# Optimization experiments

Hardware: AMD Instinct MI355X
Metric: run time of the kernel (lower is better)

## Reference

```python
import jax, jax.numpy as jnp
import numpy as np

N_NODES = 1024
N_EDGES = 32768
FEAT = 384
HID = 64
OUT = 64


def setup_inputs() -> dict:
    key = jax.random.key(0)
    ks = jax.random.split(key, 10)
    features = jax.random.normal(ks[0], (N_NODES, FEAT), dtype=jnp.float32)
    edge_index = jax.random.randint(ks[1], (2, N_EDGES), 0, N_NODES, dtype=jnp.int64 if jax.config.jax_enable_x64 else jnp.int32)
    edge_attr = jax.random.uniform(ks[2], (N_EDGES, 1), dtype=jnp.float32)
    # Linear weights (stored as [in, out]; torch Linear does x @ W.T)
    sc = 1.0 / np.sqrt(FEAT)
    Wk = jax.random.uniform(ks[3], (FEAT, HID), dtype=jnp.float32, minval=-sc, maxval=sc)
    Wq = jax.random.uniform(ks[4], (FEAT, HID), dtype=jnp.float32, minval=-sc, maxval=sc)
    Wv = jax.random.uniform(ks[5], (FEAT, OUT), dtype=jnp.float32, minval=-sc, maxval=sc)
    # Embedding tables, init N(0, 1)
    Ek = jax.random.normal(ks[6], (2, HID), dtype=jnp.float32)
    Eq = jax.random.normal(ks[7], (2, HID), dtype=jnp.float32)
    Ev = jax.random.normal(ks[8], (2, OUT), dtype=jnp.float32)
    bias = jnp.full((1,), 0.5, dtype=jnp.float32)
    mult = jnp.full((1,), 10.0, dtype=jnp.float32)
    return {"features": features, "edge_index": edge_index, "edge_attr": edge_attr,
            "Wk": Wk, "Wq": Wq, "Wv": Wv, "Ek": Ek, "Eq": Eq, "Ev": Ev,
            "bias": bias, "mult": mult}


def _dense_adj(src, dst, vals, n, d):
    # torch_geometric.utils.to_dense_adj: scatter-add edge attrs into [N, N, d]
    return jnp.zeros((n, n, d), vals.dtype).at[src, dst].add(vals)


def reference(features, edge_index, edge_attr, Wk, Wq, Wv, Ek, Eq, Ev, bias, mult):
    N, L = features.shape
    k = features @ Wk                      # [N, H]
    q = features @ Wq                      # [N, H]
    v = features @ Wv                      # [N, O]

    # ContinuousEmbeddingIndex: sigmoid interp, weights [E, 2]
    w = jax.nn.sigmoid((edge_attr - bias) * mult)
    w = jnp.concatenate([w, 1.0 - w], axis=-1)

    src, dst = edge_index[0], edge_index[1]
    A = q @ k.T                            # [N, N]

    # key relative embeddings (original casts to int64 -> truncate toward 0)
    rk = jnp.trunc(w @ Ek)                 # [E, H]
    Rk = _dense_adj(src, dst, rk, N, Ek.shape[1])
    A = A + jnp.einsum('ih,ijh->ij', q, Rk)

    # query relative embeddings (also truncated)
    rq = jnp.trunc(w @ Eq)
    Rq = _dense_adj(src, dst, rq, N, Eq.shape[1])
    A = A + jnp.einsum('jh,ijh->ij', k, Rq)

    # term3: (q_repeat * k_repeat).sum(-1) == q @ k.T again
    A = A + q @ k.T

    A = jax.nn.softmax(A / jnp.sqrt(jnp.asarray(L, A.dtype)), axis=-1)
    # dropout is identity at inference
    M = A @ v

    # value relative embeddings (float, no truncation)
    rv = w @ Ev                            # [E, O]
    Rv = _dense_adj(src, dst, rv, N, Ev.shape[1])
    M = M + jnp.einsum('ij,ijd->id', A, Rv)
    return M
```

## Files before the change

kernel.cpp:

```cpp
#include <hip/hip_runtime.h>
#include <math.h>

#define N_NODES 1024
#define N_EDGES 32768
#define FEAT    384
#define INV_S   0.05103103630798287f

__global__ __launch_bounds__(384) void k_kqv(
        const float* __restrict__ feat,
        const float* __restrict__ Wk, const float* __restrict__ Wq,
        const float* __restrict__ Wv,
        float* __restrict__ q, float* __restrict__ k, float* __restrict__ v) {
    __shared__ float fs[4 * FEAT];
    const int tid = threadIdx.x;
    const int row0 = blockIdx.x * 4;
    ((float4*)fs)[tid] = ((const float4*)(feat + (size_t)row0 * FEAT))[tid];
    __syncthreads();
    const int mat = tid >> 7;
    const int sub = tid & 127;
    const int col = sub & 63;
    const int rh  = sub >> 6;
    const float* W  = (mat == 0) ? Wq : (mat == 1 ? Wk : Wv);
    const float* f0 = fs + (rh * 2) * FEAT;
    const float* f1 = fs + (rh * 2 + 1) * FEAT;
    float a0 = 0.f, a1 = 0.f;
    #pragma unroll 8
    for (int f = 0; f < FEAT; ++f) {
        float wv = W[f * 64 + col];
        a0 = fmaf(f0[f], wv, a0);
        a1 = fmaf(f1[f], wv, a1);
    }
    float* out = (mat == 0) ? q : (mat == 1 ? k : v);
    out[(row0 + rh * 2 + 0) * 64 + col] = a0;
    out[(row0 + rh * 2 + 1) * 64 + col] = a1;
}

__global__ __launch_bounds__(256) void k_qkt(
        const float* __restrict__ q, const float* __restrict__ k,
        float* __restrict__ A) {
    __shared__ float qs[64][65];
    __shared__ float kst[64][65];
    const int tid = threadIdx.x;
    const int rowbase = blockIdx.y * 64, colbase = blockIdx.x * 64;
    for (int idx = tid; idx < 4096; idx += 256) {
        int r = idx >> 6, c = idx & 63;
        qs[r][c] = q[(rowbase + r) * 64 + c];
        kst[c][r] = k[(colbase + r) * 64 + c];
    }
    __syncthreads();
    const int tx = tid & 15, ty = tid >> 4;
    float acc[4][4] = {};
    for (int kk = 0; kk < 64; ++kk) {
        float a0 = qs[ty * 4 + 0][kk], a1 = qs[ty * 4 + 1][kk];
        float a2 = qs[ty * 4 + 2][kk], a3 = qs[ty * 4 + 3][kk];
        float b0 = kst[kk][tx * 4 + 0], b1 = kst[kk][tx * 4 + 1];
        float b2 = kst[kk][tx * 4 + 2], b3 = kst[kk][tx * 4 + 3];
        acc[0][0] = fmaf(a0, b0, acc[0][0]); acc[0][1] = fmaf(a0, b1, acc[0][1]);
        acc[0][2] = fmaf(a0, b2, acc[0][2]); acc[0][3] = fmaf(a0, b3, acc[0][3]);
        acc[1][0] = fmaf(a1, b0, acc[1][0]); acc[1][1] = fmaf(a1, b1, acc[1][1]);
        acc[1][2] = fmaf(a1, b2, acc[1][2]); acc[1][3] = fmaf(a1, b3, acc[1][3]);
        acc[2][0] = fmaf(a2, b0, acc[2][0]); acc[2][1] = fmaf(a2, b1, acc[2][1]);
        acc[2][2] = fmaf(a2, b2, acc[2][2]); acc[2][3] = fmaf(a2, b3, acc[2][3]);
        acc[3][0] = fmaf(a3, b0, acc[3][0]); acc[3][1] = fmaf(a3, b1, acc[3][1]);
        acc[3][2] = fmaf(a3, b2, acc[3][2]); acc[3][3] = fmaf(a3, b3, acc[3][3]);
    }
    for (int i = 0; i < 4; ++i) {
        float4 o = make_float4(2.f * acc[i][0], 2.f * acc[i][1],
                               2.f * acc[i][2], 2.f * acc[i][3]);
        *(float4*)&A[(size_t)(rowbase + ty * 4 + i) * N_NODES + colbase + tx * 4] = o;
    }
}

__global__ __launch_bounds__(256) void k_edgeA(
        const int* __restrict__ ei, const float* __restrict__ eattr,
        const float* __restrict__ Ek, const float* __restrict__ Eq,
        const float* __restrict__ q, const float* __restrict__ k,
        const float* __restrict__ bias, const float* __restrict__ mult,
        float* __restrict__ A) {
    const int e = (blockIdx.x * 256 + threadIdx.x) >> 6;
    const int lane = threadIdx.x & 63;
    const int src = ei[e], dst = ei[N_EDGES + e];
    const float w  = 1.0f / (1.0f + expf(-(eattr[e] - bias[0]) * mult[0]));
    const float w1 = 1.0f - w;
    const float rk = truncf(w * Ek[lane] + w1 * Ek[64 + lane]);
    const float rq = truncf(w * Eq[lane] + w1 * Eq[64 + lane]);
    float c = q[src * 64 + lane] * rk + k[dst * 64 + lane] * rq;
    #pragma unroll
    for (int off = 32; off >= 1; off >>= 1) c += __shfl_xor(c, off, 64);
    if (lane == 0) atomicAdd(&A[(size_t)src * N_NODES + dst], c);
}

__global__ __launch_bounds__(256) void k_avsm(
        const float* __restrict__ A, const float* __restrict__ v,
        float* __restrict__ rowstats, float* __restrict__ M) {
    __shared__ float As[2][1024];
    __shared__ __align__(16) float chunk[128 * 68];
    __shared__ float redm[4], reds[4];
    __shared__ float red[2][2][64];
    const int tid  = threadIdx.x;
    const int lane = tid & 63;
    const int wave = tid >> 6;
    const int row0 = blockIdx.x * 2;

    #pragma unroll
    for (int i = 0; i < 2; ++i) {
        const int idx = tid + i * 256;
        ((float4*)As)[idx] = ((const float4*)(A + (size_t)row0 * N_NODES))[idx];
    }
    __syncthreads();

    const int g  = tid >> 7;
    const int lt = tid & 127;
    {
        float4 x0 = *(float4*)&As[g][lt * 8];
        float4 x1 = *(float4*)&As[g][lt * 8 + 4];
        float m = fmaxf(fmaxf(fmaxf(x0.x, x0.y), fmaxf(x0.z, x0.w)),
                        fmaxf(fmaxf(x1.x, x1.y), fmaxf(x1.z, x1.w)));
        #pragma unroll
        for (int off = 32; off >= 1; off >>= 1) m = fmaxf(m, __shfl_xor(m, off, 64));
        if (lane == 0) redm[wave] = m;
        __syncthreads();
        m = fmaxf(redm[g * 2], redm[g * 2 + 1]);
        float e0 = expf((x0.x - m) * INV_S), e1 = expf((x0.y - m) * INV_S);
        float e2 = expf((x0.z - m) * INV_S), e3 = expf((x0.w - m) * INV_S);
        float e4 = expf((x1.x - m) * INV_S), e5 = expf((x1.y - m) * INV_S);
        float e6 = expf((x1.z - m) * INV_S), e7 = expf((x1.w - m) * INV_S);
        float s = ((e0 + e1) + (e2 + e3)) + ((e4 + e5) + (e6 + e7));
        #pragma unroll
        for (int off = 32; off >= 1; off >>= 1) s += __shfl_xor(s, off, 64);
        if (lane == 0) reds[wave] = s;
        __syncthreads();
        s = reds[g * 2] + reds[g * 2 + 1];
        const float rs = 1.0f / s;
        if (lt == 0) {
            rowstats[(row0 + g) * 2 + 0] = m;
            rowstats[(row0 + g) * 2 + 1] = rs;
        }
        *(float4*)&As[g][lt * 8]     = make_float4(e0 * rs, e1 * rs, e2 * rs, e3 * rs);
        *(float4*)&As[g][lt * 8 + 4] = make_float4(e4 * rs, e5 * rs, e6 * rs, e7 * rs);
    }
    __syncthreads();

    const int r = wave >> 1, h = wave & 1, d = lane;
    float acc = 0.f;
    for (int ch = 0; ch < 8; ++ch) {
        const int jb = ch * 128;
        #pragma unroll
        for (int it = 0; it < 8; ++it) {
            const int idx = tid + it * 256;
            const int j = idx >> 4, d4 = (idx & 15) * 4;
            *(float4*)&chunk[j * 68 + d4] =
                *(const float4*)&v[(size_t)(jb + j) * 64 + d4];
        }
        __syncthreads();
        const float* as = &As[r][jb + h * 64];
        const float* ck = &chunk[h * 64 * 68 + d];
        #pragma unroll 8
        for (int j = 0; j < 64; ++j)
            acc = fmaf(as[j], ck[j * 68], acc);
        __syncthreads();
    }
    red[r][h][d] = acc;
    __syncthreads();
    if (tid < 128) {
        const int rr = tid >> 6, dd = tid & 63;
        M[(row0 + rr) * 64 + dd] = red[rr][0][dd] + red[rr][1][dd];
    }
}

__global__ __launch_bounds__(256) void k_edgeM(
        const int* __restrict__ ei, const float* __restrict__ eattr,
        const float* __restrict__ Ev, const float* __restrict__ bias,
        const float* __restrict__ mult,
        const float* __restrict__ A, const float* __restrict__ rowstats,
        float* __restrict__ M) {
    const int e = (blockIdx.x * 256 + threadIdx.x) >> 6;
    const int lane = threadIdx.x & 63;
    const int src = ei[e], dst = ei[N_EDGES + e];
    const float logit = A[(size_t)src * N_NODES + dst];
    const float m  = rowstats[src * 2 + 0];
    const float rs = rowstats[src * 2 + 1];
    const float prob = expf((logit - m) * INV_S) * rs;
    const float w = 1.0f / (1.0f + expf(-(eattr[e] - bias[0]) * mult[0]));
    const float rv = w * Ev[lane] + (1.0f - w) * Ev[64 + lane];
    atomicAdd(&M[src * 64 + lane], prob * rv);
}

extern "C" void kernel_launch(void* const* d_in, const int* in_sizes, int n_in,
                              void* d_out, int out_size, void* d_ws, size_t ws_size,
                              hipStream_t stream) {
    (void)in_sizes; (void)n_in; (void)out_size; (void)ws_size;
    const float* feat  = (const float*)d_in[0];
    const int*   ei    = (const int*)d_in[1];
    const float* eattr = (const float*)d_in[2];
    const float* Wk    = (const float*)d_in[3];
    const float* Wq    = (const float*)d_in[4];
    const float* Wv    = (const float*)d_in[5];
    const float* Ek    = (const float*)d_in[6];
    const float* Eq    = (const float*)d_in[7];
    const float* Ev    = (const float*)d_in[8];
    const float* bias  = (const float*)d_in[9];
    const float* mult  = (const float*)d_in[10];
    float* M = (float*)d_out;

    float* wsf = (float*)d_ws;
    float* q        = wsf;
    float* k        = wsf + 65536;
    float* v        = wsf + 131072;
    float* A        = wsf + 196608;
    float* rowstats = wsf + 196608 + 1048576;

    k_kqv<<<256, 384, 0, stream>>>(feat, Wk, Wq, Wv, q, k, v);
    k_qkt<<<dim3(16, 16), 256, 0, stream>>>(q, k, A);
    k_edgeA<<<8192, 256, 0, stream>>>(ei, eattr, Ek, Eq, q, k, bias, mult, A);
    k_avsm<<<512, 256, 0, stream>>>(A, v, rowstats, M);
    k_edgeM<<<8192, 256, 0, stream>>>(ei, eattr, Ev, bias, mult, A, rowstats, M);
}
```

Before: 128.6 us.

## Factor value-embedding term into per-row scalars and restructure softmax/AV pipeline

Measured after the change: 132.2 us. 2.8% more time.

```diff
diff --git a/kernel.cpp b/kernel.cpp
--- a/kernel.cpp
+++ b/kernel.cpp
@@ -77,113 +77,130 @@
         const float* __restrict__ q, const float* __restrict__ k,
         const float* __restrict__ bias, const float* __restrict__ mult,
         float* __restrict__ A) {
-    const int e = (blockIdx.x * 256 + threadIdx.x) >> 6;
     const int lane = threadIdx.x & 63;
-    const int src = ei[e], dst = ei[N_EDGES + e];
-    const float w  = 1.0f / (1.0f + expf(-(eattr[e] - bias[0]) * mult[0]));
-    const float w1 = 1.0f - w;
-    const float rk = truncf(w * Ek[lane] + w1 * Ek[64 + lane]);
-    const float rq = truncf(w * Eq[lane] + w1 * Eq[64 + lane]);
-    float c = q[src * 64 + lane] * rk + k[dst * 64 + lane] * rq;
+    const int gw   = blockIdx.x * 4 + (threadIdx.x >> 6);
+    const float b0 = bias[0], mu = mult[0];
+    const float ek0 = Ek[lane], ek1 = Ek[64 + lane];
+    const float eq0 = Eq[lane], eq1 = Eq[64 + lane];
+    #pragma unroll 2
+    for (int i = 0; i < 4; ++i) {
+        const int e = gw + i * 8192;
+        const int src = ei[e], dst = ei[N_EDGES + e];
+        const float w  = 1.0f / (1.0f + expf(-(eattr[e] - b0) * mu));
+        const float rk = truncf(w * ek0 + (1.0f - w) * ek1);
+        const float rq = truncf(w * eq0 + (1.0f - w) * eq1);
+        float c = q[src * 64 + lane] * rk + k[dst * 64 + lane] * rq;
+        #pragma unroll
+        for (int off = 32; off >= 1; off >>= 1) c += __shfl_xor(c, off, 64);
+        if (lane == 0) atomicAdd(&A[(size_t)src * N_NODES + dst], c);
+    }
+}
+
+__global__ __launch_bounds__(256) void k_stats(
+        const float* __restrict__ A, float* __restrict__ rowstats,
+        float* __restrict__ S) {
+    const int tid = threadIdx.x, lane = tid & 63, wave = tid >> 6;
+    if (blockIdx.x == 0)
+        for (int i = tid; i < 2 * N_NODES; i += 256) S[i] = 0.f;
+    const int row = blockIdx.x * 4 + wave;
+    const float4* Ar = (const float4*)(A + (size_t)row * N_NODES);
+    float4 x0 = Ar[lane * 4 + 0], x1 = Ar[lane * 4 + 1];
+    float4 x2 = Ar[lane * 4 + 2], x3 = Ar[lane * 4 + 3];
+    float m = fmaxf(fmaxf(fmaxf(x0.x, x0.y), fmaxf(x0.z, x0.w)),
+                    fmaxf(fmaxf(x1.x, x1.y), fmaxf(x1.z, x1.w)));
+    m = fmaxf(m, fmaxf(fmaxf(fmaxf(x2.x, x2.y), fmaxf(x2.z, x2.w)),
+                       fmaxf(fmaxf(x3.x, x3.y), fmaxf(x3.z, x3.w))));
     #pragma unroll
-    for (int off = 32; off >= 1; off >>= 1) c += __shfl_xor(c, off, 64);
-    if (lane == 0) atomicAdd(&A[(size_t)src * N_NODES + dst], c);
-}
-
-__global__ __launch_bounds__(256) void k_avsm(
-        const float* __restrict__ A, const float* __restrict__ v,
-        float* __restrict__ rowstats, float* __restrict__ M) {
-    __shared__ float As[2][1024];
-    __shared__ __align__(16) float chunk[128 * 68];
-    __shared__ float redm[4], reds[4];
-    __shared__ float red[2][2][64];
-    const int tid  = threadIdx.x;
-    const int lane = tid & 63;
-    const int wave = tid >> 6;
-    const int row0 = blockIdx.x * 2;
-
+    for (int off = 32; off >= 1; off >>= 1) m = fmaxf(m, __shfl_xor(m, off, 64));
+    float s = expf((x0.x - m) * INV_S) + expf((x0.y - m) * INV_S)
+            + expf((x0.z - m) * INV_S) + expf((x0.w - m) * INV_S)
+            + expf((x1.x - m) * INV_S) + expf((x1.y - m) * INV_S)
+            + expf((x1.z - m) * INV_S) + expf((x1.w - m) * INV_S)
+            + expf((x2.x - m) * INV_S) + expf((x2.y - m) * INV_S)
+            + expf((x2.z - m) * INV_S) + expf((x2.w - m) * INV_S)
+            + expf((x3.x - m) * INV_S) + expf((x3.y - m) * INV_S)
+            + expf((x3.z - m) * INV_S) + expf((x3.w - m) * INV_S);
     #pragma unroll
-    for (int i = 0; i < 2; ++i) {
-        const int idx = tid + i * 256;
-        ((float4*)As)[idx] = ((const float4*)(A + (size_t)row0 * N_NODES))[idx];
-    }
-    __syncthreads();
-
-    const int g  = tid >> 7;
-    const int lt = tid & 127;
-    {
-        float4 x0 = *(float4*)&As[g][lt * 8];
-        float4 x1 = *(float4*)&As[g][lt * 8 + 4];
-        float m = fmaxf(fmaxf(fmaxf(x0.x, x0.y), fmaxf(x0.z, x0.w)),
-                        fmaxf(fmaxf(x1.x, x1.y), fmaxf(x1.z, x1.w)));
-        #pragma unroll
-        for (int off = 32; off >= 1; off >>= 1) m = fmaxf(m, __shfl_xor(m, off, 64));
-        if (lane == 0) redm[wave] = m;
-        __syncthreads();
-        m = fmaxf(redm[g * 2], redm[g * 2 + 1]);
-        float e0 = expf((x0.x - m) * INV_S), e1 = expf((x0.y - m) * INV_S);
-        float e2 = expf((x0.z - m) * INV_S), e3 = expf((x0.w - m) * INV_S);
-        float e4 = expf((x1.x - m) * INV_S), e5 = expf((x1.y - m) * INV_S);
-        float e6 = expf((x1.z - m) * INV_S), e7 = expf((x1.w - m) * INV_S);
-        float s = ((e0 + e1) + (e2 + e3)) + ((e4 + e5) + (e6 + e7));
-        #pragma unroll
-        for (int off = 32; off >= 1; off >>= 1) s += __shfl_xor(s, off, 64);
-        if (lane == 0) reds[wave] = s;
-        __syncthreads();
-        s = reds[g * 2] + reds[g * 2 + 1];
-        const float rs = 1.0f / s;
-        if (lt == 0) {
-            rowstats[(row0 + g) * 2 + 0] = m;
-            rowstats[(row0 + g) * 2 + 1] = rs;
-        }
-        *(float4*)&As[g][lt * 8]     = make_float4(e0 * rs, e1 * rs, e2 * rs, e3 * rs);
-        *(float4*)&As[g][lt * 8 + 4] = make_float4(e4 * rs, e5 * rs, e6 * rs, e7 * rs);
-    }
-    __syncthreads();
-
-    const int r = wave >> 1, h = wave & 1, d = lane;
-    float acc = 0.f;
-    for (int ch = 0; ch < 8; ++ch) {
-        const int jb = ch * 128;
-        #pragma unroll
-        for (int it = 0; it < 8; ++it) {
-            const int idx = tid + it * 256;
-            const int j = idx >> 4, d4 = (idx & 15) * 4;
-            *(float4*)&chunk[j * 68 + d4] =
-                *(const float4*)&v[(size_t)(jb + j) * 64 + d4];
-        }
-        __syncthreads();
-        const float* as = &As[r][jb + h * 64];
-        const float* ck = &chunk[h * 64 * 68 + d];
-        #pragma unroll 8
-        for (int j = 0; j < 64; ++j)
-            acc = fmaf(as[j], ck[j * 68], acc);
-        __syncthreads();
-    }
-    red[r][h][d] = acc;
-    __syncthreads();
-    if (tid < 128) {
-        const int rr = tid >> 6, dd = tid & 63;
-        M[(row0 + rr) * 64 + dd] = red[rr][0][dd] + red[rr][1][dd];
-    }
-}
-
-__global__ __launch_bounds__(256) void k_edgeM(
+    for (int off = 32; off >= 1; off >>= 1) s += __shfl_xor(s, off, 64);
+    if (lane == 0) {
+        rowstats[row * 2 + 0] = m;
+        rowstats[row * 2 + 1] = 1.0f / s;
+    }
+}
+
+__global__ __launch_bounds__(256) void k_edgeS(
         const int* __restrict__ ei, const float* __restrict__ eattr,
-        const float* __restrict__ Ev, const float* __restrict__ bias,
-        const float* __restrict__ mult,
         const float* __restrict__ A, const float* __restrict__ rowstats,
-        float* __restrict__ M) {
-    const int e = (blockIdx.x * 256 + threadIdx.x) >> 6;
-    const int lane = threadIdx.x & 63;
+        const float* __restrict__ bias, const float* __restrict__ mult,
+        float* __restrict__ S) {
+    const int e = blockIdx.x * 256 + threadIdx.x;
     const int src = ei[e], dst = ei[N_EDGES + e];
     const float logit = A[(size_t)src * N_NODES + dst];
     const float m  = rowstats[src * 2 + 0];
     const float rs = rowstats[src * 2 + 1];
     const float prob = expf((logit - m) * INV_S) * rs;
     const float w = 1.0f / (1.0f + expf(-(eattr[e] - bias[0]) * mult[0]));
-    const float rv = w * Ev[lane] + (1.0f - w) * Ev[64 + lane];
-    atomicAdd(&M[src * 64 + lane], prob * rv);
+    atomicAdd(&S[src * 2 + 0], prob * w);
+    atomicAdd(&S[src * 2 + 1], prob * (1.0f - w));
+}
+
+__global__ __launch_bounds__(256) void k_av(
+        const float* __restrict__ A, const float* __restrict__ v,
+        const float* __restrict__ rowstats, const float* __restrict__ S,
+        const float* __restrict__ Ev, float* __restrict__ M) {
+    __shared__ float P[2][1024];
+    __shared__ float red[2][4][64];
+    const int tid  = threadIdx.x;
+    const int lane = tid & 63;
+    const int wave = tid >> 6;
+    const int row0 = blockIdx.x * 2;
+
+    {
+        const int g  = tid >> 7;
+        const int lt = tid & 127;
+        const float m  = rowstats[(row0 + g) * 2 + 0];
+        const float rs = rowstats[(row0 + g) * 2 + 1];
+        const float4* Ar = (const float4*)(A + (size_t)(row0 + g) * N_NODES);
+        float4 x0 = Ar[lt * 2], x1 = Ar[lt * 2 + 1];
+        *(float4*)&P[g][lt * 8] = make_float4(
+            expf((x0.x - m) * INV_S) * rs, expf((x0.y - m) * INV_S) * rs,
+            expf((x0.z - m) * INV_S) * rs, expf((x0.w - m) * INV_S) * rs);
+        *(float4*)&P[g][lt * 8 + 4] = make_float4(
+            expf((x1.x - m) * INV_S) * rs, expf((x1.y - m) * INV_S) * rs,
+            expf((x1.z - m) * INV_S) * rs, expf((x1.w - m) * INV_S) * rs);
+    }
+    __syncthreads();
+
+    {
+        const float* vp = v + (size_t)(wave * 256) * 64 + lane;
+        const float* p0 = &P[0][wave * 256];
+        const float* p1 = &P[1][wave * 256];
+        float acc0 = 0.f, acc1 = 0.f;
+        #pragma unroll 2
+        for (int j4 = 0; j4 < 256; j4 += 4) {
+            float4 a0 = *(const float4*)&p0[j4];
+            float4 a1 = *(const float4*)&p1[j4];
+            float v0 = vp[(j4 + 0) * 64];
+            float v1 = vp[(j4 + 1) * 64];
+            float v2 = vp[(j4 + 2) * 64];
+            float v3 = vp[(j4 + 3) * 64];
+            acc0 = fmaf(a0.x, v0, acc0); acc0 = fmaf(a0.y, v1, acc0);
+            acc0 = fmaf(a0.z, v2, acc0); acc0 = fmaf(a0.w, v3, acc0);
+            acc1 = fmaf(a1.x, v0, acc1); acc1 = fmaf(a1.y, v1, acc1);
+            acc1 = fmaf(a1.z, v2, acc1); acc1 = fmaf(a1.w, v3, acc1);
+        }
+        red[0][wave][lane] = acc0;
+        red[1][wave][lane] = acc1;
+    }
+    __syncthreads();
+
+    if (tid < 128) {
+        const int r = tid >> 6, d = tid & 63;
+        const int row = row0 + r;
+        float acc = (red[r][0][d] + red[r][1][d]) + (red[r][2][d] + red[r][3][d]);
+        acc += S[row * 2 + 0] * Ev[d] + S[row * 2 + 1] * Ev[64 + d];
+        M[row * 64 + d] = acc;
+    }
 }
 
 extern "C" void kernel_launch(void* const* d_in, const int* in_sizes, int n_in,
@@ -209,10 +226,12 @@
     float* v        = wsf + 131072;
     float* A        = wsf + 196608;
     float* rowstats = wsf + 196608 + 1048576;
+    float* S        = rowstats + 2048;
 
     k_kqv<<<256, 384, 0, stream>>>(feat, Wk, Wq, Wv, q, k, v);
     k_qkt<<<dim3(16, 16), 256, 0, stream>>>(q, k, A);
-    k_edgeA<<<8192, 256, 0, stream>>>(ei, eattr, Ek, Eq, q, k, bias, mult, A);
-    k_avsm<<<512, 256, 0, stream>>>(A, v, rowstats, M);
-    k_edgeM<<<8192, 256, 0, stream>>>(ei, eattr, Ev, bias, mult, A, rowstats, M);
-}
+    k_edgeA<<<2048, 256, 0, stream>>>(ei, eattr, Ek, Eq, q, k, bias, mult, A);
+    k_stats<<<256, 256, 0, stream>>>(A, rowstats, S);
+    k_edgeS<<<128, 256, 0, stream>>>(ei, eattr, A, rowstats, bias, mult, S);
+    k_av<<<512, 256, 0, stream>>>(A, v, rowstats, S, Ev, M);
+}
```

## Fuse edge scatter, softmax, AV and edge-value terms into one row-block kernel

Applied to the files above, without the earlier changes.

Measured after the change: 123.8 us. 1.04x faster.

```diff
diff --git a/kernel.cpp b/kernel.cpp
--- a/kernel.cpp
+++ b/kernel.cpp
@@ -5,6 +5,7 @@
 #define N_EDGES 32768
 #define FEAT    384
 #define INV_S   0.05103103630798287f
+#define MAXH    1024
 
 __global__ __launch_bounds__(384) void k_kqv(
         const float* __restrict__ feat,
@@ -71,41 +72,73 @@
     }
 }
 
-__global__ __launch_bounds__(256) void k_edgeA(
+__global__ __launch_bounds__(512) void k_mega(
+        const float* __restrict__ A0, const float* __restrict__ q,
+        const float* __restrict__ k, const float* __restrict__ v,
         const int* __restrict__ ei, const float* __restrict__ eattr,
         const float* __restrict__ Ek, const float* __restrict__ Eq,
-        const float* __restrict__ q, const float* __restrict__ k,
+        const float* __restrict__ Ev,
         const float* __restrict__ bias, const float* __restrict__ mult,
-        float* __restrict__ A) {
-    const int e = (blockIdx.x * 256 + threadIdx.x) >> 6;
-    const int lane = threadIdx.x & 63;
-    const int src = ei[e], dst = ei[N_EDGES + e];
-    const float w  = 1.0f / (1.0f + expf(-(eattr[e] - bias[0]) * mult[0]));
-    const float w1 = 1.0f - w;
-    const float rk = truncf(w * Ek[lane] + w1 * Ek[64 + lane]);
-    const float rq = truncf(w * Eq[lane] + w1 * Eq[64 + lane]);
-    float c = q[src * 64 + lane] * rk + k[dst * 64 + lane] * rq;
-    #pragma unroll
-    for (int off = 32; off >= 1; off >>= 1) c += __shfl_xor(c, off, 64);
-    if (lane == 0) atomicAdd(&A[(size_t)src * N_NODES + dst], c);
-}
-
-__global__ __launch_bounds__(256) void k_avsm(
-        const float* __restrict__ A, const float* __restrict__ v,
-        float* __restrict__ rowstats, float* __restrict__ M) {
-    __shared__ float As[2][1024];
-    __shared__ __align__(16) float chunk[128 * 68];
-    __shared__ float redm[4], reds[4];
-    __shared__ float red[2][2][64];
+        float* __restrict__ M) {
+    __shared__ __align__(16) float As[4][N_NODES];
+    __shared__ float qr[4][64];
+    __shared__ __align__(16) float scratch[2048];
+    __shared__ float redm[8], reds[8];
+    __shared__ float sS[4][2];
+    __shared__ int nhit;
+    int*   list  = (int*)scratch;
+    float* wlist = scratch + 1024;
+    float* red   = scratch;
+
     const int tid  = threadIdx.x;
     const int lane = tid & 63;
     const int wave = tid >> 6;
-    const int row0 = blockIdx.x * 2;
-
-    #pragma unroll
-    for (int i = 0; i < 2; ++i) {
-        const int idx = tid + i * 256;
-        ((float4*)As)[idx] = ((const float4*)(A + (size_t)row0 * N_NODES))[idx];
+    const int row0 = blockIdx.x * 4;
+
+    if (tid < 8) ((float*)sS)[tid] = 0.f;
+    if (tid == 8) nhit = 0;
+    __syncthreads();
+
+    {
+        const float4* src4 = (const float4*)(A0 + (size_t)row0 * N_NODES);
+        #pragma unroll
+        for (int i = 0; i < 2; ++i)
+            ((float4*)As)[tid + i * 512] = src4[tid + i * 512];
+        if (tid < 256) qr[tid >> 6][tid & 63] = q[row0 * 64 + tid];
+
+        const int4* s4 = (const int4*)ei;
+        #pragma unroll 4
+        for (int it = 0; it < 16; ++it) {
+            const int i4 = tid + it * 512;
+            const int4 sv = s4[i4];
+            const int eb = i4 * 4;
+            if ((unsigned)(sv.x - row0) < 4u) { int p = atomicAdd(&nhit, 1); if (p < MAXH) list[p] = eb + 0; }
+            if ((unsigned)(sv.y - row0) < 4u) { int p = atomicAdd(&nhit, 1); if (p < MAXH) list[p] = eb + 1; }
+            if ((unsigned)(sv.z - row0) < 4u) { int p = atomicAdd(&nhit, 1); if (p < MAXH) list[p] = eb + 2; }
+            if ((unsigned)(sv.w - row0) < 4u) { int p = atomicAdd(&nhit, 1); if (p < MAXH) list[p] = eb + 3; }
+        }
+    }
+    __syncthreads();
+    const int nh = min(nhit, MAXH);
+
+    {
+        const float b0 = bias[0], mu = mult[0];
+        const float ek0 = Ek[lane], ek1 = Ek[64 + lane];
+        const float eq0 = Eq[lane], eq1 = Eq[64 + lane];
+        for (int i = wave; i < nh; i += 8) {
+            const int e   = list[i];
+            const int src = ei[e], dst = ei[N_EDGES + e];
+            const float w  = 1.0f / (1.0f + expf(-(eattr[e] - b0) * mu));
+            const float rk = truncf(w * ek0 + (1.0f - w) * ek1);
+            const float rq = truncf(w * eq0 + (1.0f - w) * eq1);
+            float c = qr[src - row0][lane] * rk + k[(size_t)dst * 64 + lane] * rq;
+            #pragma unroll
+            for (int off = 32; off >= 1; off >>= 1) c += __shfl_xor(c, off, 64);
+            if (lane == 0) {
+                atomicAdd(&As[src - row0][dst], c);
+                wlist[i] = w;
+            }
+        }
     }
     __syncthreads();
 
@@ -132,58 +165,61 @@
         __syncthreads();
         s = reds[g * 2] + reds[g * 2 + 1];
         const float rs = 1.0f / s;
-        if (lt == 0) {
-            rowstats[(row0 + g) * 2 + 0] = m;
-            rowstats[(row0 + g) * 2 + 1] = rs;
-        }
         *(float4*)&As[g][lt * 8]     = make_float4(e0 * rs, e1 * rs, e2 * rs, e3 * rs);
         *(float4*)&As[g][lt * 8 + 4] = make_float4(e4 * rs, e5 * rs, e6 * rs, e7 * rs);
     }
     __syncthreads();
 
-    const int r = wave >> 1, h = wave & 1, d = lane;
-    float acc = 0.f;
-    for (int ch = 0; ch < 8; ++ch) {
-        const int jb = ch * 128;
-        #pragma unroll
-        for (int it = 0; it < 8; ++it) {
-            const int idx = tid + it * 256;
-            const int j = idx >> 4, d4 = (idx & 15) * 4;
-            *(float4*)&chunk[j * 68 + d4] =
-                *(const float4*)&v[(size_t)(jb + j) * 64 + d4];
+    for (int i = tid; i < nh; i += 512) {
+        const int e  = list[i];
+        const int rl = ei[e] - row0, dst = ei[N_EDGES + e];
+        const float pr = As[rl][dst];
+        const float w  = wlist[i];
+        atomicAdd(&sS[rl][0], pr * w);
+        atomicAdd(&sS[rl][1], pr * (1.0f - w));
+    }
+    __syncthreads();
+
+    {
+        const float* vp = v + (size_t)(wave * 128) * 64 + lane;
+        const float* p0 = &As[0][wave * 128];
+        const float* p1 = &As[1][wave * 128];
+        const float* p2 = &As[2][wave * 128];
+        const float* p3 = &As[3][wave * 128];
+        float a0 = 0.f, a1 = 0.f, a2 = 0.f, a3 = 0.f;
+        #pragma unroll 2
+        for (int j4 = 0; j4 < 128; j4 += 4) {
+            float4 c0 = *(const float4*)&p0[j4];
+            float4 c1 = *(const float4*)&p1[j4];
+            float4 c2 = *(const float4*)&p2[j4];
+            float4 c3 = *(const float4*)&p3[j4];
+            float v0 = vp[(j4 + 0) * 64];
+            float v1 = vp[(j4 + 1) * 64];
+            float v2 = vp[(j4 + 2) * 64];
+            float v3 = vp[(j4 + 3) * 64];
+            a0 = fmaf(c0.x, v0, a0); a0 = fmaf(c0.y, v1, a0);
+            a0 = fmaf(c0.z, v2, a0); a0 = fmaf(c0.w, v3, a0);
+            a1 = fmaf(c1.x, v0, a1); a1 = fmaf(c1.y, v1, a1);
+            a1 = fmaf(c1.z, v2, a1); a1 = fmaf(c1.w, v3, a1);
+            a2 = fmaf(c2.x, v0, a2); a2 = fmaf(c2.y, v1, a2);
+            a2 = fmaf(c2.z, v2, a2); a2 = fmaf(c2.w, v3, a2);
+            a3 = fmaf(c3.x, v0, a3); a3 = fmaf(c3.y, v1, a3);
+            a3 = fmaf(c3.z, v2, a3); a3 = fmaf(c3.w, v3, a3);
         }
-        __syncthreads();
-        const float* as = &As[r][jb + h * 64];
-        const float* ck = &chunk[h * 64 * 68 + d];
-        #pragma unroll 8
-        for (int j = 0; j < 64; ++j)
-            acc = fmaf(as[j], ck[j * 68], acc);
-        __syncthreads();
-    }
-    red[r][h][d] = acc;
-    __syncthreads();
-    if (tid < 128) {
-        const int rr = tid >> 6, dd = tid & 63;
-        M[(row0 + rr) * 64 + dd] = red[rr][0][dd] + red[rr][1][dd];
-    }
-}
-
-__global__ __launch_bounds__(256) void k_edgeM(
-        const int* __restrict__ ei, const float* __restrict__ eattr,
-        const float* __restrict__ Ev, const float* __restrict__ bias,
-        const float* __restrict__ mult,
-        const float* __restrict__ A, const float* __restrict__ rowstats,
-        float* __restrict__ M) {
-    const int e = (blockIdx.x * 256 + threadIdx.x) >> 6;
-    const int lane = threadIdx.x & 63;
-    const int src = ei[e], dst = ei[N_EDGES + e];
-    const float logit = A[(size_t)src * N_NODES + dst];
-    const float m  = rowstats[src * 2 + 0];
-    const float rs = rowstats[src * 2 + 1];
-    const float prob = expf((logit - m) * INV_S) * rs;
-    const float w = 1.0f / (1.0f + expf(-(eattr[e] - bias[0]) * mult[0]));
-    const float rv = w * Ev[lane] + (1.0f - w) * Ev[64 + lane];
-    atomicAdd(&M[src * 64 + lane], prob * rv);
+        red[(0 * 8 + wave) * 64 + lane] = a0;
+        red[(1 * 8 + wave) * 64 + lane] = a1;
+        red[(2 * 8 + wave) * 64 + lane] = a2;
+        red[(3 * 8 + wave) * 64 + lane] = a3;
+    }
+    __syncthreads();
+    if (tid < 256) {
+        const int r = tid >> 6, d = tid & 63;
+        float acc = 0.f;
+        #pragma unroll
+        for (int w8 = 0; w8 < 8; ++w8) acc += red[(r * 8 + w8) * 64 + d];
+        acc += sS[r][0] * Ev[d] + sS[r][1] * Ev[64 + d];
+        M[(row0 + r) * 64 + d] = acc;
+    }
 }
 
 extern "C" void kernel_launch(void* const* d_in, const int* in_sizes, int n_in,
@@ -204,15 +240,13 @@
     float* M = (float*)d_out;
 
     float* wsf = (float*)d_ws;
-    float* q        = wsf;
-    float* k        = wsf + 65536;
-    float* v        = wsf + 131072;
-    float* A        = wsf + 196608;
-    float* rowstats = wsf + 196608 + 1048576;
+    float* q = wsf;
+    float* k = wsf + 65536;
+    float* v = wsf + 131072;
+    float* A = wsf + 196608;
 
     k_kqv<<<256, 384, 0, stream>>>(feat, Wk, Wq, Wv, q, k, v);
     k_qkt<<<dim3(16, 16), 256, 0, stream>>>(q, k, A);
-    k_edgeA<<<8192, 256, 0, stream>>>(ei, eattr, Ek, Eq, q, k, bias, mult, A);
-    k_avsm<<<512, 256, 0, stream>>>(A, v, rowstats, M);
-    k_edgeM<<<8192, 256, 0, stream>>>(ei, eattr, Ev, bias, mult, A, rowstats, M);
-}
+    k_mega<<<256, 512, 0, stream>>>(A, q, k, v, ei, eattr, Ek, Eq, Ev,
+                                    bias, mult, M);
+}
```
